# Kernel optimization log

Hardware: AMD Instinct MI355X
Metric: run time of the kernel (lower is better)

The kernel has to match this reference:

```python
import jax, jax.numpy as jnp
import numpy as np

# dims: B batch, T frames, N tokens/frame, C embed, H heads, D=C//H, MEM memory slots
B, T, N, C = 8, 16, 196, 768
H = 8
D = C // H
MEM = 196          # mem_size; with N=196 -> _init_t = 1, M stays == MEM
HID = 4 * C        # mlp_ratio * embed_dim
STD = 0.02


def _mlp(x, w1, b1, w2, b2):
    # timm-style Mlp: fc1 -> GELU -> fc2 (dropout = 0)
    return jax.nn.gelu(x @ w1 + b1, approximate=False) @ w2 + b2


def _ln(x, w, b, eps=1e-5):
    mu = jnp.mean(x, axis=-1, keepdims=True)
    var = jnp.var(x, axis=-1, keepdims=True)
    return (x - mu) * jax.lax.rsqrt(var + eps) * w + b


def setup_inputs() -> dict:
    key = jax.random.key(0)
    ks = jax.random.split(key, 10)
    f32 = jnp.float32
    return {
        "cur_fea": jax.random.normal(ks[0], (B, T, N, C), f32),
        "norm1_w": jnp.ones((C,), f32), "norm1_b": jnp.zeros((C,), f32),
        "norm2_w": jnp.ones((C,), f32), "norm2_b": jnp.zeros((C,), f32),
        # c_func: Mlp(2C -> 4C -> C)
        "c_w1": jax.random.normal(ks[1], (2 * C, HID), f32) * STD, "c_b1": jnp.zeros((HID,), f32),
        "c_w2": jax.random.normal(ks[2], (HID, C), f32) * STD, "c_b2": jnp.zeros((C,), f32),
        # m_func: Mlp(C -> 4C -> C)
        "m_w1": jax.random.normal(ks[3], (C, HID), f32) * STD, "m_b1": jnp.zeros((HID,), f32),
        "m_w2": jax.random.normal(ks[4], (HID, C), f32) * STD, "m_b2": jnp.zeros((C,), f32),
        # post_func: Mlp(C -> 4C -> C)
        "p_w1": jax.random.normal(ks[5], (C, HID), f32) * STD, "p_b1": jnp.zeros((HID,), f32),
        "p_w2": jax.random.normal(ks[6], (HID, C), f32) * STD, "p_b2": jnp.zeros((C,), f32),
        # ProjectDotDistance: per-head q(c_global) . k(mem) * scale -> sigmoid
        "q_w": jax.random.normal(ks[7], (C, C), f32) * STD, "q_b": jnp.zeros((C,), f32),
        "k_w": jax.random.normal(ks[8], (C, C), f32) * STD, "k_b": jnp.zeros((C,), f32),
    }


def reference(cur_fea, norm1_w, norm1_b, norm2_w, norm2_b,
              c_w1, c_b1, c_w2, c_b2, m_w1, m_b1, m_w2, m_b2,
              p_w1, p_b1, p_w2, p_b2, q_w, q_b, k_w, k_b):
    x = _ln(cur_fea, norm1_w, norm1_b)                       # [B,T,N,C]
    # T*N > mem_size, _init_t = MEM // N = 1 -> init memory = frame 0 (no grad, torch.no_grad)
    init_mem = jax.lax.stop_gradient(x[:, 0].reshape(B, MEM, C))
    scale = D ** -0.5

    def step(mem, fea):                                      # mem [B,MEM,C], fea [B,N,C]
        ap = jnp.mean(mem, axis=1, keepdims=True)            # [B,1,C]
        cg = _mlp(jnp.concatenate([fea, jnp.broadcast_to(ap, fea.shape)], axis=-1),
                  c_w1, c_b1, c_w2, c_b2)                    # [B,N,C]
        memh = _mlp(mem, m_w1, m_b1, m_w2, m_b2).reshape(B, MEM, H, D).transpose(0, 2, 1, 3)  # [B,H,M,D]
        q = (cg @ q_w + q_b).reshape(B, N, H, D).transpose(0, 2, 1, 3)    # [B,H,N,D]
        k = (mem @ k_w + k_b).reshape(B, MEM, H, D).transpose(0, 2, 1, 3) # [B,H,M,D]
        o = jax.nn.sigmoid(jnp.einsum('bhnd,bhmd->bhnm', q, k) * scale)   # [B,H,N,M]
        cgh = cg.reshape(B, N, H, D).transpose(0, 2, 1, 3)               # [B,H,N,D]
        c = jnp.einsum('bhnm,bhnd->bmhd', o, cgh).reshape(B, MEM, C)
        c = _mlp(c, p_w1, p_b1, p_w2, p_b2)
        # mean_N((1-o) * broadcast(memh)) == mean_N(1-o) * memh (memh indep of N)
        gate = jnp.mean(1.0 - o, axis=2)                     # [B,H,M]
        og = (gate[..., None] * memh).transpose(0, 2, 1, 3).reshape(B, MEM, C)
        new_mem = _ln(c + og, norm2_w, norm2_b)
        return new_mem, None

    fea_seq = x[:, 1:].transpose(1, 0, 2, 3)                 # [T-1,B,N,C]
    final_mem, _ = jax.lax.scan(step, init_mem, fea_seq)
    return final_mem                                         # [B,MEM,C]
```

## Files before the change

kernel.cpp:

```cpp
#include <hip/hip_runtime.h>
#include <hip/hip_bf16.h>
#include <math.h>

constexpr int B_   = 8;
constexpr int T_   = 16;
constexpr int N_   = 196;
constexpr int C_   = 768;
constexpr int H_   = 8;
constexpr int D_   = 96;
constexpr int M_   = 196;
constexpr int HID_ = 3072;
constexpr int ROWS_ = B_ * N_;
constexpr int MP_   = 1664;

typedef __hip_bfloat16 bf16;
typedef __attribute__((ext_vector_type(8))) short bf16x8;
typedef __attribute__((ext_vector_type(4))) float f32x4;

__device__ __forceinline__ float b2f(bf16 x) { return __bfloat162float(x); }
__device__ __forceinline__ short bf2s(bf16 x) { union { bf16 b; short s; } u; u.b = x; return u.s; }
__device__ __forceinline__ float s2f(short x) { union { bf16 b; short s; } u; u.s = x; return __bfloat162float(u.b); }

#define GL2LDS(g, l) __builtin_amdgcn_global_load_lds( \
    (__attribute__((address_space(1))) void*)(g), \
    (__attribute__((address_space(3))) void*)(l), 16, 0, 0)

__device__ __forceinline__ void hard_barrier() {
    asm volatile("" ::: "memory");
    __builtin_amdgcn_s_barrier();
    asm volatile("" ::: "memory");
}


__device__ __forceinline__ float block_reduce_sum256(float v, float* sdata) {
    int tid = threadIdx.x;
    sdata[tid] = v;
    __syncthreads();
    for (int s = 128; s > 0; s >>= 1) {
        if (tid < s) sdata[tid] += sdata[tid + s];
        __syncthreads();
    }
    float r = sdata[0];
    __syncthreads();
    return r;
}

struct TEnt { const float* W; bf16* Wt; int K; int N; int tiles; };
struct TEnts { TEnt e[8]; };

__global__ __launch_bounds__(256) void transpose_all_kernel(TEnts tds)
{
    __shared__ float tile[32][33];
    int local = blockIdx.x;
    int i = 0;
    while (i < 7 && local >= tds.e[i].tiles) { local -= tds.e[i].tiles; ++i; }
    TEnt g = tds.e[i];
    int ntx = g.N / 32;
    int n0 = (local % ntx) * 32, k0 = (local / ntx) * 32;
    int tx = threadIdx.x & 31, ty = threadIdx.x >> 5;
#pragma unroll
    for (int r = 0; r < 32; r += 8)
        tile[ty + r][tx] = g.W[(size_t)(k0 + ty + r) * g.N + n0 + tx];
    __syncthreads();
#pragma unroll
    for (int r = 0; r < 32; r += 8)
        g.Wt[(size_t)(n0 + ty + r) * g.K + k0 + tx] = __float2bfloat16(tile[tx][ty + r]);
}

__global__ __launch_bounds__(256) void cvt_kernel(const float* __restrict__ W,
                                                  bf16* __restrict__ o, int n)
{
    int i = blockIdx.x * 256 + threadIdx.x;
    if (i < n) o[i] = __float2bfloat16(W[i]);
}

__global__ __launch_bounds__(256) void ln_frame_kernel(
    const float* __restrict__ cur, int t,
    const float* __restrict__ w, const float* __restrict__ bia,
    bf16* __restrict__ mem_bf)
{
    __shared__ float sdata[256];
    int row = blockIdx.x;
    int b = row / N_, n = row % N_;
    const float* src = cur + (((size_t)b * T_ + t) * N_ + n) * C_;
    float x[3];
    float sum = 0.f, sumsq = 0.f;
#pragma unroll
    for (int i = 0; i < 3; i++) {
        int c = threadIdx.x + i * 256;
        x[i] = src[c];
        sum += x[i]; sumsq += x[i] * x[i];
    }
    sum = block_reduce_sum256(sum, sdata);
    sumsq = block_reduce_sum256(sumsq, sdata);
    float mu = sum * (1.0f / C_);
    float var = sumsq * (1.0f / C_) - mu * mu;
    float rs = rsqrtf(var + 1e-5f);
#pragma unroll
    for (int i = 0; i < 3; i++) {
        int c = threadIdx.x + i * 256;
        mem_bf[(size_t)row * C_ + c] = __float2bfloat16((x[i] - mu) * rs * w[c] + bia[c]);
    }
}

__global__ __launch_bounds__(256) void ap_partial_kernel(const bf16* __restrict__ mem,
                                                         float* __restrict__ app)
{
    int ch = blockIdx.x, b = blockIdx.y;
    int m0 = ch * 25;
    int m1 = m0 + 25; if (m1 > M_) m1 = M_;
    const bf16* p = mem + (size_t)b * M_ * C_;
#pragma unroll
    for (int i = 0; i < 3; i++) {
        int c = threadIdx.x + i * 256;
        float s = 0.f;
        for (int m = m0; m < m1; m++) s += b2f(p[(size_t)m * C_ + c]);
        app[((size_t)b * 8 + ch) * C_ + c] = s;
    }
}

__global__ __launch_bounds__(256) void build_cat_kernel(
    const float* __restrict__ cur, int t,
    const float* __restrict__ w, const float* __restrict__ bia,
    const float* __restrict__ app, bf16* __restrict__ cat)
{
    __shared__ float sdata[256];
    int row = blockIdx.x;
    int b = row / N_, n = row % N_;
    const float* src = cur + (((size_t)b * T_ + t) * N_ + n) * C_;
    float x[3];
    float sum = 0.f, sumsq = 0.f;
#pragma unroll
    for (int i = 0; i < 3; i++) {
        int c = threadIdx.x + i * 256;
        x[i] = src[c];
        sum += x[i]; sumsq += x[i] * x[i];
    }
    sum = block_reduce_sum256(sum, sdata);
    sumsq = block_reduce_sum256(sumsq, sdata);
    float mu = sum * (1.0f / C_);
    float var = sumsq * (1.0f / C_) - mu * mu;
    float rs = rsqrtf(var + 1e-5f);
    bf16* dstrow = cat + (size_t)row * (2 * C_);
#pragma unroll
    for (int i = 0; i < 3; i++) {
        int c = threadIdx.x + i * 256;
        dstrow[c] = __float2bfloat16((x[i] - mu) * rs * w[c] + bia[c]);
        float apv = 0.f;
#pragma unroll
        for (int j = 0; j < 8; j++) apv += app[((size_t)b * 8 + j) * C_ + c];
        dstrow[C_ + c] = __float2bfloat16(apv * (1.0f / M_));
    }
}

struct GemmDesc {
    const bf16* A; const bf16* W; const float* bias; bf16* out;
    int K; int N; int ymax; int gelu;
};
struct GemmDescs { GemmDesc d[4]; };

template <int BN>
__global__ __launch_bounds__(256) void mfma_gemm_multi(GemmDescs ds)
{
    constexpr int BM = 128;
    constexpr int TI = 4;
    constexpr int TJ = (BN / 2) / 16;
    constexpr int ABYTES = BM * 128;
    constexpr int BBYTES = BN * 128;
    constexpr int AR = ABYTES / 4096;
    constexpr int BR = BBYTES / 4096;
    __shared__ short As[BM * 64];
    __shared__ short Bs[BN * 64];

    GemmDesc g = ds.d[blockIdx.z];
    if ((int)blockIdx.y >= g.ymax) return;

    int tid = threadIdx.x;
    int wid = tid >> 6;
    int lane = tid & 63;
    int quad = lane >> 4, l15 = lane & 15;
    int row0 = blockIdx.x * BM;
    int col0 = blockIdx.y * BN;
    int wm = (wid >> 1) * 64;
    int wn = (wid & 1) * (BN / 2);

    f32x4 acc[TI][TJ] = {};

    const char* Ab = (const char*)g.A;
    const char* Wb = (const char*)g.W;
    const size_t Kb = (size_t)g.K * 2;
    const int base = wid * 1024;

    auto stage = [&](int k0) {
        char* Ad = (char*)As;
        char* Bd = (char*)Bs;
#pragma unroll
        for (int r = 0; r < AR; r++) {
            int o = r * 4096 + base + lane * 16;
            int row = o >> 7, cs = (o >> 4) & 7;
            int kc = cs ^ (row & 7);
            GL2LDS(Ab + (size_t)(row0 + row) * Kb + (size_t)k0 * 2 + kc * 16, Ad + o);
        }
#pragma unroll
        for (int r = 0; r < BR; r++) {
            int o = r * 4096 + base + lane * 16;
            int row = o >> 7, cs = (o >> 4) & 7;
            int kc = cs ^ (row & 7);
            GL2LDS(Wb + (size_t)(col0 + row) * Kb + (size_t)k0 * 2 + kc * 16, Bd + o);
        }
    };

    const int nk = g.K / 64;
    for (int ki = 0; ki < nk; ki++) {
        stage(ki * 64);
        asm volatile("s_waitcnt vmcnt(0)" ::: "memory");
        hard_barrier();
        const bf16x8* Av = (const bf16x8*)As;
        const bf16x8* Bv = (const bf16x8*)Bs;
        bf16x8 af[TI][2], bfr[TJ][2];
#pragma unroll
        for (int i = 0; i < TI; i++) {
            int r = wm + i * 16 + l15;
#pragma unroll
            for (int hh = 0; hh < 2; hh++)
                af[i][hh] = Av[r * 8 + ((hh * 4 + quad) ^ (r & 7))];
        }
#pragma unroll
        for (int j = 0; j < TJ; j++) {
            int r = wn + j * 16 + l15;
#pragma unroll
            for (int hh = 0; hh < 2; hh++)
                bfr[j][hh] = Bv[r * 8 + ((hh * 4 + quad) ^ (r & 7))];
        }
#pragma unroll
        for (int hh = 0; hh < 2; hh++)
#pragma unroll
            for (int i = 0; i < TI; i++)
#pragma unroll
                for (int j = 0; j < TJ; j++)
                    acc[i][j] = __builtin_amdgcn_mfma_f32_16x16x32_bf16(
                        af[i][hh], bfr[j][hh], acc[i][j], 0, 0, 0);
        hard_barrier();
    }

#pragma unroll
    for (int i = 0; i < TI; i++) {
        int gr = row0 + wm + i * 16 + quad * 4;
#pragma unroll
        for (int j = 0; j < TJ; j++) {
            int gc = col0 + wn + j * 16 + l15;
            float bv = g.bias ? g.bias[gc] : 0.0f;
#pragma unroll
            for (int r = 0; r < 4; r++) {
                float v = acc[i][j][r] + bv;
                if (g.gelu) v = 0.5f * v * (1.0f + erff(v * 0.7071067811865475f));
                g.out[(size_t)(gr + r) * g.N + gc] = __float2bfloat16(v);
            }
        }
    }
}

__global__ __launch_bounds__(256) void mfma_gemm_splitk(
    const bf16* __restrict__ A, const bf16* __restrict__ Wt,
    float* __restrict__ part, int K)
{
    constexpr int BM = 128;
    constexpr int BN = 64;
    constexpr int TI = 4;
    constexpr int TJ = 2;
    constexpr int AR = 4, BR = 2;
    __shared__ short As[BM * 64];
    __shared__ short Bs[BN * 64];

    int tid = threadIdx.x;
    int wid = tid >> 6;
    int lane = tid & 63;
    int quad = lane >> 4, l15 = lane & 15;
    int row0 = blockIdx.x * BM;
    int col0 = blockIdx.y * BN;
    int wm = (wid >> 1) * 64;
    int wn = (wid & 1) * 32;
    int kh = K >> 1;
    int kbeg = blockIdx.z * kh;

    f32x4 acc[TI][TJ] = {};
    const char* Ab = (const char*)A;
    const char* Wb = (const char*)Wt;
    const size_t Kb = (size_t)K * 2;
    const int base = wid * 1024;

    auto stage = [&](int k0) {
        char* Ad = (char*)As;
        char* Bd = (char*)Bs;
#pragma unroll
        for (int r = 0; r < AR; r++) {
            int o = r * 4096 + base + lane * 16;
            int row = o >> 7, cs = (o >> 4) & 7;
            int kc = cs ^ (row & 7);
            GL2LDS(Ab + (size_t)(row0 + row) * Kb + (size_t)k0 * 2 + kc * 16, Ad + o);
        }
#pragma unroll
        for (int r = 0; r < BR; r++) {
            int o = r * 4096 + base + lane * 16;
            int row = o >> 7, cs = (o >> 4) & 7;
            int kc = cs ^ (row & 7);
            GL2LDS(Wb + (size_t)(col0 + row) * Kb + (size_t)k0 * 2 + kc * 16, Bd + o);
        }
    };

    const int nk = kh / 64;
    for (int ki = 0; ki < nk; ki++) {
        stage(kbeg + ki * 64);
        asm volatile("s_waitcnt vmcnt(0)" ::: "memory");
        hard_barrier();
        const bf16x8* Av = (const bf16x8*)As;
        const bf16x8* Bv = (const bf16x8*)Bs;
        bf16x8 af[TI][2], bfr[TJ][2];
#pragma unroll
        for (int i = 0; i < TI; i++) {
            int r = wm + i * 16 + l15;
#pragma unroll
            for (int hh = 0; hh < 2; hh++)
                af[i][hh] = Av[r * 8 + ((hh * 4 + quad) ^ (r & 7))];
        }
#pragma unroll
        for (int j = 0; j < TJ; j++) {
            int r = wn + j * 16 + l15;
#pragma unroll
            for (int hh = 0; hh < 2; hh++)
                bfr[j][hh] = Bv[r * 8 + ((hh * 4 + quad) ^ (r & 7))];
        }
#pragma unroll
        for (int hh = 0; hh < 2; hh++)
#pragma unroll
            for (int i = 0; i < TI; i++)
#pragma unroll
                for (int j = 0; j < TJ; j++)
                    acc[i][j] = __builtin_amdgcn_mfma_f32_16x16x32_bf16(
                        af[i][hh], bfr[j][hh], acc[i][j], 0, 0, 0);
        hard_barrier();
    }

    float* outp = part + (size_t)blockIdx.z * MP_ * C_;
#pragma unroll
    for (int i = 0; i < TI; i++) {
        int gr = row0 + wm + i * 16 + quad * 4;
#pragma unroll
        for (int j = 0; j < TJ; j++) {
            int gc = col0 + wn + j * 16 + l15;
#pragma unroll
            for (int r = 0; r < 4; r++)
                outp[(size_t)(gr + r) * C_ + gc] = acc[i][j][r];
        }
    }
}

__global__ __launch_bounds__(256) void b2q_kernel(
    const float* __restrict__ c_b2, const float* __restrict__ q_b,
    const bf16* __restrict__ W2q_t, float* __restrict__ b2q)
{
    __shared__ float sdata[256];
    int n = blockIdx.x;
    const bf16* row = W2q_t + (size_t)n * HID_;
    float s = 0.f;
    for (int j = threadIdx.x; j < HID_; j += 256) s += c_b2[j] * b2f(row[j]);
    s = block_reduce_sum256(s, sdata);
    if (threadIdx.x == 0) b2q[n] = s + q_b[n];
}

__global__ __launch_bounds__(512) void attn_mfma_kernel(
    const bf16* __restrict__ q, const bf16* __restrict__ k,
    const bf16* __restrict__ cg, bf16* __restrict__ cbuf,
    float* __restrict__ gate)
{
    constexpr int KS = 104;
    constexpr int PSS = 40;
    __shared__ short Ks[64 * KS];
    __shared__ short Qs[32 * KS];
    __shared__ short CGt[96 * PSS];
    __shared__ short Ph[64 * PSS];
    __shared__ short Pl[64 * PSS];
    __shared__ float gred[8][64];

    const int mt = blockIdx.x, h = blockIdx.y, b = blockIdx.z;
    const int m0 = (mt < 3) ? mt * 64 : (M_ - 64);
    const int tid = threadIdx.x;
    const int w = tid >> 6, lane = tid & 63;
    const int quad = lane >> 4, l15 = lane & 15;
    const int wm = w >> 1;
    const int wh = w & 1;
    const float scale = 0.10206207261596575f;

    const bf16* qp = q  + (size_t)b * N_ * C_ + h * D_;
    const bf16* kp = k  + (size_t)b * M_ * C_ + h * D_;
    const bf16* cp = cg + (size_t)b * N_ * C_ + h * D_;

    for (int idx = tid; idx < 64 * 12; idx += 512) {
        int r = idx / 12, c = idx % 12;
        *(bf16x8*)(Ks + r * KS + c * 8) =
            *(const bf16x8*)(kp + (size_t)(m0 + r) * C_ + c * 8);
    }

    f32x4 acc[3] = {};
    float gacc = 0.f;

    const bf16x8 ZEROV = {0, 0, 0, 0, 0, 0, 0, 0};
    bf16x8 qv = ZEROV, cgv = ZEROV;
    const bool active = tid < 32 * 12;
    const int qrow = tid / 12, qcol = (tid % 12) * 8;
    const int cgn = tid & 31, cgd = (tid >> 5) * 8;

    auto issue = [&](int n0) {
        if (!active) return;
        int nq = n0 + qrow;
        qv = (nq < N_) ? *(const bf16x8*)(qp + (size_t)nq * C_ + qcol) : ZEROV;
        int nc = n0 + cgn;
        cgv = (nc < N_) ? *(const bf16x8*)(cp + (size_t)nc * C_ + cgd) : ZEROV;
    };
    auto stage = [&]() {
        if (!active) return;
        *(bf16x8*)(Qs + qrow * KS + qcol) = qv;
#pragma unroll
        for (int i = 0; i < 8; i++) CGt[(cgd + i) * PSS + cgn] = cgv[i];
    };

    issue(0);
    for (int nt = 0; nt < 7; nt++) {
        stage();
        __syncthreads();
        if (nt < 6) issue((nt + 1) * 32);

        f32x4 s4 = {};
#pragma unroll
        for (int kk = 0; kk < 3; kk++) {
            bf16x8 af = *(const bf16x8*)(Ks + (wm * 16 + l15) * KS + kk * 32 + quad * 8);
            bf16x8 bq = *(const bf16x8*)(Qs + (wh * 16 + l15) * KS + kk * 32 + quad * 8);
            s4 = __builtin_amdgcn_mfma_f32_16x16x32_bf16(af, bq, s4, 0, 0, 0);
        }
        const int nglob = nt * 32 + wh * 16 + l15;
#pragma unroll
        for (int r = 0; r < 4; r++) {
            float p = (nglob < N_) ? 1.f / (1.f + expf(-s4[r] * scale)) : 0.f;
            bf16 hb = __float2bfloat16(p);
            bf16 lb = __float2bfloat16(p - __bfloat162float(hb));
            int po = (wm * 16 + quad * 4 + r) * PSS + wh * 16 + l15;
            Ph[po] = bf2s(hb);
            Pl[po] = bf2s(lb);
        }
        __syncthreads();

        {
            const short* ph = Ph + lane * PSS + w * 4;
            const short* pl = Pl + lane * PSS + w * 4;
#pragma unroll
            for (int u = 0; u < 4; u++) gacc += s2f(ph[u]) + s2f(pl[u]);
        }
        bf16x8 pa = *(const bf16x8*)(Ph + (wm * 16 + l15) * PSS + quad * 8);
        bf16x8 pb = *(const bf16x8*)(Pl + (wm * 16 + l15) * PSS + quad * 8);
#pragma unroll
        for (int dt = 0; dt < 3; dt++) {
            bf16x8 bcg = *(const bf16x8*)(CGt + (wh * 48 + dt * 16 + l15) * PSS + quad * 8);
            acc[dt] = __builtin_amdgcn_mfma_f32_16x16x32_bf16(pa, bcg, acc[dt], 0, 0, 0);
            acc[dt] = __builtin_amdgcn_mfma_f32_16x16x32_bf16(pb, bcg, acc[dt], 0, 0, 0);
        }
        __syncthreads();
    }

#pragma unroll
    for (int dt = 0; dt < 3; dt++)
#pragma unroll
        for (int r = 0; r < 4; r++) {
            int m = m0 + wm * 16 + quad * 4 + r;
            cbuf[((size_t)b * M_ + m) * C_ + h * D_ + wh * 48 + dt * 16 + l15] =
                __float2bfloat16(acc[dt][r]);
        }
    gred[w][lane] = gacc;
    __syncthreads();
    if (tid < 64) {
        float g = 0.f;
#pragma unroll
        for (int s = 0; s < 8; s++) g += gred[s][tid];
        gate[((size_t)b * H_ + h) * M_ + m0 + tid] = 1.f - g * (1.0f / N_);
    }
}

__global__ __launch_bounds__(256) void final_kernel(
    const float* __restrict__ part, const float* __restrict__ p_b2,
    const float* __restrict__ gate, const bf16* __restrict__ memh,
    const float* __restrict__ w, const float* __restrict__ bia,
    bf16* __restrict__ mem_bf, float* __restrict__ outp)
{
    __shared__ float sdata[256];
    int row = blockIdx.x;
    int b = row / M_, m = row % M_;
    float x[3];
    float sum = 0.f, sumsq = 0.f;
#pragma unroll
    for (int i = 0; i < 3; i++) {
        int c = threadIdx.x + i * 256;
        int h = c / D_;
        float v = part[(size_t)row * C_ + c] + part[(size_t)MP_ * C_ + (size_t)row * C_ + c]
                + p_b2[c]
                + gate[(b * H_ + h) * M_ + m] * b2f(memh[(size_t)row * C_ + c]);
        x[i] = v;
        sum += v; sumsq += v * v;
    }
    sum = block_reduce_sum256(sum, sdata);
    sumsq = block_reduce_sum256(sumsq, sdata);
    float mu = sum * (1.0f / C_);
    float var = sumsq * (1.0f / C_) - mu * mu;
    float rs = rsqrtf(var + 1e-5f);
#pragma unroll
    for (int i = 0; i < 3; i++) {
        int c = threadIdx.x + i * 256;
        float v = (x[i] - mu) * rs * w[c] + bia[c];
        mem_bf[(size_t)row * C_ + c] = __float2bfloat16(v);
        if (outp) outp[(size_t)row * C_ + c] = v;
    }
}

extern "C" void kernel_launch(void* const* d_in, const int* in_sizes, int n_in,
                              void* d_out, int out_size, void* d_ws, size_t ws_size,
                              hipStream_t stream)
{
    const float* cur_fea = (const float*)d_in[0];
    const float* n1w = (const float*)d_in[1];
    const float* n1b = (const float*)d_in[2];
    const float* n2w = (const float*)d_in[3];
    const float* n2b = (const float*)d_in[4];
    const float* c_w1 = (const float*)d_in[5];
    const float* c_b1 = (const float*)d_in[6];
    const float* c_w2 = (const float*)d_in[7];
    const float* c_b2 = (const float*)d_in[8];
    const float* m_w1 = (const float*)d_in[9];
    const float* m_b1 = (const float*)d_in[10];
    const float* m_w2 = (const float*)d_in[11];
    const float* m_b2 = (const float*)d_in[12];
    const float* p_w1 = (const float*)d_in[13];
    const float* p_b1 = (const float*)d_in[14];
    const float* p_w2 = (const float*)d_in[15];
    const float* p_b2 = (const float*)d_in[16];
    const float* q_w = (const float*)d_in[17];
    const float* q_b = (const float*)d_in[18];
    const float* k_w = (const float*)d_in[19];
    const float* k_b = (const float*)d_in[20];

    size_t off = 0;
    char* base = (char*)d_ws;
    auto carve = [&](size_t bytes) -> char* {
        char* r = base + off;
        off += (bytes + 255) & ~(size_t)255;
        return r;
    };
    bf16* cw1t = (bf16*)carve((size_t)HID_ * (2 * C_) * 2);
    bf16* cw2t = (bf16*)carve((size_t)C_ * HID_ * 2);
    bf16* mw1t = (bf16*)carve((size_t)HID_ * C_ * 2);
    bf16* mw2t = (bf16*)carve((size_t)C_ * HID_ * 2);
    bf16* pw1t = (bf16*)carve((size_t)HID_ * C_ * 2);
    bf16* pw2t = (bf16*)carve((size_t)C_ * HID_ * 2);
    bf16* qwt  = (bf16*)carve((size_t)C_ * C_ * 2);
    bf16* kwt  = (bf16*)carve((size_t)C_ * C_ * 2);
    bf16* mem_bf = (bf16*)carve((size_t)MP_ * C_ * 2);
    char* catreg = carve((size_t)MP_ * 2 * C_ * 2);
    bf16* cat = (bf16*)catreg;
    bf16* qb  = (bf16*)catreg;
    bf16* kb  = (bf16*)catreg + (size_t)MP_ * C_;
    bf16* hid_c = (bf16*)carve((size_t)MP_ * HID_ * 2);
    char* hidm_reg = carve((size_t)MP_ * HID_ * 2);
    bf16*  hid_m = (bf16*)hidm_reg;
    float* part  = (float*)hidm_reg;
    bf16* cg    = (bf16*)carve((size_t)MP_ * C_ * 2);
    bf16* cbuf  = (bf16*)carve((size_t)MP_ * C_ * 2);
    bf16* memh  = (bf16*)carve((size_t)MP_ * C_ * 2);
    float* app  = (float*)carve((size_t)B_ * 8 * C_ * 4);
    float* gateb = (float*)carve((size_t)B_ * H_ * M_ * 4);
    float* b2qb  = (float*)carve((size_t)C_ * 4);
    bf16* W2q_t = (bf16*)carve((size_t)C_ * HID_ * 2);
    const bool fuse_q = (off <= ws_size);

    const dim3 blk(256);

    {
        TEnts tds;
        tds.e[0] = { c_w1, cw1t, 2 * C_, HID_, (HID_ / 32) * ((2 * C_) / 32) };
        tds.e[1] = { c_w2, cw2t, HID_, C_, (C_ / 32) * (HID_ / 32) };
        tds.e[2] = { m_w1, mw1t, C_, HID_, (HID_ / 32) * (C_ / 32) };
        tds.e[3] = { m_w2, mw2t, HID_, C_, (C_ / 32) * (HID_ / 32) };
        tds.e[4] = { p_w1, pw1t, C_, HID_, (HID_ / 32) * (C_ / 32) };
        tds.e[5] = { p_w2, pw2t, HID_, C_, (C_ / 32) * (HID_ / 32) };
        tds.e[6] = { q_w, qwt, C_, C_, (C_ / 32) * (C_ / 32) };
        tds.e[7] = { k_w, kwt, C_, C_, (C_ / 32) * (C_ / 32) };
        int total = 4608 + 2304 * 5 + 576 * 2;
        transpose_all_kernel<<<total, blk, 0, stream>>>(tds);
    }

    if (fuse_q) {
        bf16* cw2nt = hid_c;
        cvt_kernel<<<(HID_ * C_ + 255) / 256, blk, 0, stream>>>(c_w2, cw2nt, HID_ * C_);
        GemmDescs ds;
        ds.d[0] = { qwt, cw2nt, nullptr, W2q_t, C_, HID_, HID_ / 128, 0 };
        ds.d[1] = ds.d[0]; ds.d[2] = ds.d[0]; ds.d[3] = ds.d[0];
        mfma_gemm_multi<128><<<dim3(C_ / 128, HID_ / 128, 1), blk, 0, stream>>>(ds);
        b2q_kernel<<<C_, blk, 0, stream>>>(c_b2, q_b, W2q_t, b2qb);
    }

    ln_frame_kernel<<<ROWS_, blk, 0, stream>>>(cur_fea, 0, n1w, n1b, mem_bf);

    for (int t = 1; t < T_; t++) {
        ap_partial_kernel<<<dim3(8, B_), blk, 0, stream>>>(mem_bf, app);
        build_cat_kernel<<<ROWS_, blk, 0, stream>>>(cur_fea, t, n1w, n1b, app, cat);

        {
            GemmDescs ds;
            ds.d[0] = { cat,    cw1t, c_b1, hid_c, 2 * C_, HID_, HID_ / 128, 1 };
            ds.d[1] = { mem_bf, mw1t, m_b1, hid_m, C_,     HID_, HID_ / 128, 1 };
            ds.d[2] = ds.d[0]; ds.d[3] = ds.d[0];
            mfma_gemm_multi<128><<<dim3(MP_ / 128, HID_ / 128, 2), blk, 0, stream>>>(ds);
        }
        {
            GemmDescs ds;
            ds.d[0] = { hid_c,  cw2t, c_b2, cg,   HID_, C_, C_ / 64, 0 };
            ds.d[1] = { hid_m,  mw2t, m_b2, memh, HID_, C_, C_ / 64, 0 };
            ds.d[2] = { mem_bf, kwt,  k_b,  kb,   C_,   C_, C_ / 64, 0 };
            ds.d[3] = { hid_c,  W2q_t, b2qb, qb,  HID_, C_, C_ / 64, 0 };
            mfma_gemm_multi<64><<<dim3(MP_ / 128, C_ / 64, fuse_q ? 4 : 3), blk, 0, stream>>>(ds);
        }
        if (!fuse_q) {
            GemmDescs ds;
            ds.d[0] = { cg, qwt, q_b, qb, C_, C_, C_ / 64, 0 };
            ds.d[1] = ds.d[0]; ds.d[2] = ds.d[0]; ds.d[3] = ds.d[0];
            mfma_gemm_multi<64><<<dim3(MP_ / 128, C_ / 64, 1), blk, 0, stream>>>(ds);
        }
        attn_mfma_kernel<<<dim3(4, H_, B_), dim3(512), 0, stream>>>(qb, kb, cg, cbuf, gateb);
        {
            GemmDescs ds;
            ds.d[0] = { cbuf, pw1t, p_b1, hid_c, C_, HID_, HID_ / 64, 1 };
            ds.d[1] = ds.d[0]; ds.d[2] = ds.d[0]; ds.d[3] = ds.d[0];
            mfma_gemm_multi<64><<<dim3(MP_ / 128, HID_ / 64, 1), blk, 0, stream>>>(ds);
        }
        mfma_gemm_splitk<<<dim3(MP_ / 128, C_ / 64, 2), blk, 0, stream>>>(hid_c, pw2t, part, HID_);
        final_kernel<<<ROWS_, blk, 0, stream>>>(part, p_b2, gateb, memh, n2w, n2b,
                                                mem_bf, (t == T_ - 1) ? (float*)d_out : nullptr);
    }
}
```

Before: 3.090 ms.

## Multi-buffer LDS staging in MFMA GEMMs to overlap loads with compute

Turns the single-buffered LDS tiles of the multi-GEMM and split-K GEMM kernels into double- or triple-buffered rings. Global-to-LDS loads for the next one or two K-steps are issued ahead, and a partial vmcnt wait covers only the current tile. The goal is to hide global memory latency behind the MFMA work instead of stalling on every K-step. The cost is more LDS per block (up to 72KB for the triple-buffered BN=64 tiles), which can reduce occupancy.

```diff
diff --git a/kernel.cpp b/kernel.cpp
--- a/kernel.cpp
+++ b/kernel.cpp
@@ -77,7 +77,7 @@
 __global__ __launch_bounds__(256) void ln_frame_kernel(
     const float* __restrict__ cur, int t,
     const float* __restrict__ w, const float* __restrict__ bia,
-    bf16* __restrict__ mem_bf)
+    bf16* __restrict__ dst)
 {
     __shared__ float sdata[256];
     int row = blockIdx.x;
@@ -99,7 +99,7 @@
 #pragma unroll
     for (int i = 0; i < 3; i++) {
         int c = threadIdx.x + i * 256;
-        mem_bf[(size_t)row * C_ + c] = __float2bfloat16((x[i] - mu) * rs * w[c] + bia[c]);
+        dst[(size_t)row * C_ + c] = __float2bfloat16((x[i] - mu) * rs * w[c] + bia[c]);
     }
 }
 
@@ -159,7 +159,7 @@
 };
 struct GemmDescs { GemmDesc d[4]; };
 
-template <int BN>
+template <int BN, int NBUF>
 __global__ __launch_bounds__(256) void mfma_gemm_multi(GemmDescs ds)
 {
     constexpr int BM = 128;
@@ -169,8 +169,9 @@
     constexpr int BBYTES = BN * 128;
     constexpr int AR = ABYTES / 4096;
     constexpr int BR = BBYTES / 4096;
-    __shared__ short As[BM * 64];
-    __shared__ short Bs[BN * 64];
+    constexpr int NL = AR + BR;
+    __shared__ short As[NBUF * BM * 64];
+    __shared__ short Bs[NBUF * BN * 64];
 
     GemmDesc g = ds.d[blockIdx.z];
     if ((int)blockIdx.y >= g.ymax) return;
@@ -191,9 +192,9 @@
     const size_t Kb = (size_t)g.K * 2;
     const int base = wid * 1024;
 
-    auto stage = [&](int k0) {
-        char* Ad = (char*)As;
-        char* Bd = (char*)Bs;
+    auto stage = [&](int k0, int sel) {
+        char* Ad = (char*)As + sel * ABYTES;
+        char* Bd = (char*)Bs + sel * BBYTES;
 #pragma unroll
         for (int r = 0; r < AR; r++) {
             int o = r * 4096 + base + lane * 16;
@@ -211,12 +212,19 @@
     };
 
     const int nk = g.K / 64;
+    stage(0, 0);
+    if (NBUF == 3 && nk > 1) stage(64, 1);
     for (int ki = 0; ki < nk; ki++) {
-        stage(ki * 64);
-        asm volatile("s_waitcnt vmcnt(0)" ::: "memory");
+        int sel = ki % NBUF;
+        constexpr int AHEAD = NBUF - 1;
+        if (ki + AHEAD < nk) stage((ki + AHEAD) * 64, (ki + AHEAD) % NBUF);
+        int pend = nk - 1 - ki; if (pend > AHEAD) pend = AHEAD;
+        if (pend >= 2)      asm volatile("s_waitcnt vmcnt(%0)" :: "n"(2 * NL) : "memory");
+        else if (pend == 1) asm volatile("s_waitcnt vmcnt(%0)" :: "n"(NL) : "memory");
+        else                asm volatile("s_waitcnt vmcnt(0)" ::: "memory");
         hard_barrier();
-        const bf16x8* Av = (const bf16x8*)As;
-        const bf16x8* Bv = (const bf16x8*)Bs;
+        const bf16x8* Av = (const bf16x8*)(As + sel * BM * 64);
+        const bf16x8* Bv = (const bf16x8*)(Bs + sel * BN * 64);
         bf16x8 af[TI][2], bfr[TJ][2];
 #pragma unroll
         for (int i = 0; i < TI; i++) {
@@ -268,9 +276,11 @@
     constexpr int BN = 64;
     constexpr int TI = 4;
     constexpr int TJ = 2;
-    constexpr int AR = 4, BR = 2;
-    __shared__ short As[BM * 64];
-    __shared__ short Bs[BN * 64];
+    constexpr int ABYTES = BM * 128, BBYTES = BN * 128;
+    constexpr int AR = 4, BR = 2, NL = 6;
+    constexpr int NBUF = 3;
+    __shared__ short As[NBUF * BM * 64];
+    __shared__ short Bs[NBUF * BN * 64];
 
     int tid = threadIdx.x;
     int wid = tid >> 6;
@@ -289,9 +299,9 @@
     const size_t Kb = (size_t)K * 2;
     const int base = wid * 1024;
 
-    auto stage = [&](int k0) {
-        char* Ad = (char*)As;
-        char* Bd = (char*)Bs;
+    auto stage = [&](int k0, int sel) {
+        char* Ad = (char*)As + sel * ABYTES;
+        char* Bd = (char*)Bs + sel * BBYTES;
 #pragma unroll
         for (int r = 0; r < AR; r++) {
             int o = r * 4096 + base + lane * 16;
@@ -309,12 +319,18 @@
     };
 
     const int nk = kh / 64;
+    stage(kbeg, 0);
+    if (nk > 1) stage(kbeg + 64, 1);
     for (int ki = 0; ki < nk; ki++) {
-        stage(kbeg + ki * 64);
-        asm volatile("s_waitcnt vmcnt(0)" ::: "memory");
+        int sel = ki % NBUF;
+        if (ki + 2 < nk) stage(kbeg + (ki + 2) * 64, (ki + 2) % NBUF);
+        int pend = nk - 1 - ki; if (pend > 2) pend = 2;
+        if (pend >= 2)      asm volatile("s_waitcnt vmcnt(%0)" :: "n"(2 * NL) : "memory");
+        else if (pend == 1) asm volatile("s_waitcnt vmcnt(%0)" :: "n"(NL) : "memory");
+        else                asm volatile("s_waitcnt vmcnt(0)" ::: "memory");
         hard_barrier();
-        const bf16x8* Av = (const bf16x8*)As;
-        const bf16x8* Bv = (const bf16x8*)Bs;
+        const bf16x8* Av = (const bf16x8*)(As + sel * BM * 64);
+        const bf16x8* Bv = (const bf16x8*)(Bs + sel * BN * 64);
         bf16x8 af[TI][2], bfr[TJ][2];
 #pragma unroll
         for (int i = 0; i < TI; i++) {
@@ -600,7 +616,7 @@
         GemmDescs ds;
         ds.d[0] = { qwt, cw2nt, nullptr, W2q_t, C_, HID_, HID_ / 128, 0 };
         ds.d[1] = ds.d[0]; ds.d[2] = ds.d[0]; ds.d[3] = ds.d[0];
-        mfma_gemm_multi<128><<<dim3(C_ / 128, HID_ / 128, 1), blk, 0, stream>>>(ds);
+        mfma_gemm_multi<128, 2><<<dim3(C_ / 128, HID_ / 128, 1), blk, 0, stream>>>(ds);
         b2q_kernel<<<C_, blk, 0, stream>>>(c_b2, q_b, W2q_t, b2qb);
     }
 
@@ -615,7 +631,7 @@
             ds.d[0] = { cat,    cw1t, c_b1, hid_c, 2 * C_, HID_, HID_ / 128, 1 };
             ds.d[1] = { mem_bf, mw1t, m_b1, hid_m, C_,     HID_, HID_ / 128, 1 };
             ds.d[2] = ds.d[0]; ds.d[3] = ds.d[0];
-            mfma_gemm_multi<128><<<dim3(MP_ / 128, HID_ / 128, 2), blk, 0, stream>>>(ds);
+            mfma_gemm_multi<128, 2><<<dim3(MP_ / 128, HID_ / 128, 2), blk, 0, stream>>>(ds);
         }
         {
             GemmDescs ds;
@@ -623,20 +639,20 @@
             ds.d[1] = { hid_m,  mw2t, m_b2, memh, HID_, C_, C_ / 64, 0 };
             ds.d[2] = { mem_bf, kwt,  k_b,  kb,   C_,   C_, C_ / 64, 0 };
             ds.d[3] = { hid_c,  W2q_t, b2qb, qb,  HID_, C_, C_ / 64, 0 };
-            mfma_gemm_multi<64><<<dim3(MP_ / 128, C_ / 64, fuse_q ? 4 : 3), blk, 0, stream>>>(ds);
+            mfma_gemm_multi<64, 3><<<dim3(MP_ / 128, C_ / 64, fuse_q ? 4 : 3), blk, 0, stream>>>(ds);
         }
         if (!fuse_q) {
             GemmDescs ds;
             ds.d[0] = { cg, qwt, q_b, qb, C_, C_, C_ / 64, 0 };
             ds.d[1] = ds.d[0]; ds.d[2] = ds.d[0]; ds.d[3] = ds.d[0];
-            mfma_gemm_multi<64><<<dim3(MP_ / 128, C_ / 64, 1), blk, 0, stream>>>(ds);
+            mfma_gemm_multi<64, 3><<<dim3(MP_ / 128, C_ / 64, 1), blk, 0, stream>>>(ds);
         }
         attn_mfma_kernel<<<dim3(4, H_, B_), dim3(512), 0, stream>>>(qb, kb, cg, cbuf, gateb);
         {
             GemmDescs ds;
             ds.d[0] = { cbuf, pw1t, p_b1, hid_c, C_, HID_, HID_ / 64, 1 };
             ds.d[1] = ds.d[0]; ds.d[2] = ds.d[0]; ds.d[3] = ds.d[0];
-            mfma_gemm_multi<64><<<dim3(MP_ / 128, HID_ / 64, 1), blk, 0, stream>>>(ds);
+            mfma_gemm_multi<64, 3><<<dim3(MP_ / 128, HID_ / 64, 1), blk, 0, stream>>>(ds);
         }
         mfma_gemm_splitk<<<dim3(MP_ / 128, C_ / 64, 2), blk, 0, stream>>>(hid_c, pw2t, part, HID_);
         final_kernel<<<ROWS_, blk, 0, stream>>>(part, p_b2, gateb, memh, n2w, n2b,
```

Result: slower. 3.468 ms (+12.2%).
